# Kernel optimization log

Measured on AMD Instinct MI355X. Metric: run time of the kernel, lower is better.

The kernel has to match this reference:

```python
import jax, jax.numpy as jnp
import numpy as np


def setup_inputs() -> dict:
    key = jax.random.key(0)
    B, S = 8, 4096
    MAX_SEQ_LEN = 4096
    D_MODEL = 1024
    # ids are float in [0, max_seq_len); original module casts int ids to float anyway
    input_ids = jax.random.uniform(key, (B, S), dtype=jnp.float32) * MAX_SEQ_LEN
    return {"input_ids": input_ids, "max_seq_len": MAX_SEQ_LEN, "d_model": D_MODEL}


def reference(input_ids, max_seq_len, d_model):
    # Normalize ids from [0, max_seq_len] to [-1, 1] (Chebyshev domain).
    x = 2.0 * input_ids.astype(jnp.float32) / max_seq_len - 1.0  # [B, S]
    t0 = jnp.ones_like(x)  # T_0(x) = 1
    t1 = x                  # T_1(x) = x

    def step(carry, _):
        t_prev, t_cur = carry
        t_next = 2.0 * x * t_cur - t_prev
        return (t_cur, t_next), t_next

    _, rest = jax.lax.scan(step, (t0, t1), None, length=d_model - 2)
    # rest: [d_model-2, B, S]
    emb = jnp.concatenate([t0[None], t1[None], rest], axis=0)  # [d_model, B, S]
    return jnp.moveaxis(emb, 0, -1)  # [B, S, d_model]
```

## Files before the change

### kernel.cpp

```cpp
#include <hip/hip_runtime.h>
#include <hip/hip_bf16.h>

__global__ void __launch_bounds__(256)
cheb_kernel(const float* __restrict__ ids,
            const int* __restrict__ p_maxlen,
            float* __restrict__ out,
            int n_rows, int d_model) {
    const float inv = 2.0f / (float)(*p_maxlen);
    const int per_row = d_model >> 3;
    const long long total = (long long)n_rows * per_row;
    const long long stride = (long long)gridDim.x * blockDim.x;
    for (long long tid = (long long)blockIdx.x * blockDim.x + threadIdx.x;
         tid < total; tid += stride) {
        const int row = (int)(tid / per_row);
        const int seg = (int)(tid - (long long)row * per_row);

        float x = fmaf(ids[row], inv, -1.0f);
        x = fminf(fmaxf(x, -1.0f), 1.0f);
        const float sx = sqrtf(fmaxf(0.0f, 1.0f - x * x));
        const float theta = acosf(x);

        const int n0 = seg << 3;
        float c, s;
        sincosf((float)n0 * theta, &s, &c);

        float v[8];
#pragma unroll
        for (int k = 0; k < 8; ++k) {
            v[k] = c;
            const float nc = fmaf(c, x, -(s * sx));
            const float ns = fmaf(s, x,  (c * sx));
            c = nc; s = ns;
        }

        float4* o = (float4*)(out + tid * 8);
        o[0] = make_float4(v[0], v[1], v[2], v[3]);
        o[1] = make_float4(v[4], v[5], v[6], v[7]);
    }
}

extern "C" void kernel_launch(void* const* d_in, const int* in_sizes, int n_in,
                              void* d_out, int out_size, void* d_ws, size_t ws_size,
                              hipStream_t stream) {
    const float* ids     = (const float*)d_in[0];
    const int*   pmaxlen = (const int*)d_in[1];
    float*       out     = (float*)d_out;

    const int n_rows  = in_sizes[0];
    const int d_model = out_size / n_rows;

    const long long total = (long long)n_rows * (d_model >> 3);
    int blocks = (int)((total + 255) / 256);
    if (blocks > 16384) blocks = 16384;

    cheb_kernel<<<blocks, 256, 0, stream>>>(ids, pmaxlen, out, n_rows, d_model);
}
```

Baseline: 31.22 us.

## Specialize d_model=1024 path with one wave per row and coalesced stores

Adds a kernel specialized for d_model=1024. Each wavefront handles one row, and each lane writes float4s at lane-contiguous addresses across four 256-element chunks, so stores are fully coalesced. The base angles come from the hardware sin/cos instructions on revolution-scaled, range-reduced inputs, and a rotation recurrence steps between chunks instead of calling sincosf per segment. This trades some accuracy from the native trig and the longer recurrence for cheaper math and better store patterns. Other d_model values fall back to the generic kernel.

```diff
diff --git a/kernel.cpp b/kernel.cpp
--- a/kernel.cpp
+++ b/kernel.cpp
@@ -1,11 +1,57 @@
 #include <hip/hip_runtime.h>
 #include <hip/hip_bf16.h>
 
+#define INV2PI 0.15915494309189535f
+
 __global__ void __launch_bounds__(256)
-cheb_kernel(const float* __restrict__ ids,
-            const int* __restrict__ p_maxlen,
-            float* __restrict__ out,
-            int n_rows, int d_model) {
+cheb1024_kernel(const float* __restrict__ ids,
+                const int* __restrict__ p_maxlen,
+                float* __restrict__ out,
+                int n_rows) {
+    const float inv = 2.0f / (float)(*p_maxlen);
+    const int wave = threadIdx.x >> 6;
+    const int lane = threadIdx.x & 63;
+    const int row  = blockIdx.x * 4 + wave;
+    if (row >= n_rows) return;
+
+    float x = fmaf(ids[row], inv, -1.0f);
+    x = fminf(fmaxf(x, -1.0f), 1.0f);
+    const float sx = sqrtf(fmaxf(0.0f, 1.0f - x * x));
+    const float trev = acosf(x) * INV2PI;
+
+    float brev = (float)(4 * lane) * trev;
+    brev -= floorf(brev);
+    float bc = __builtin_amdgcn_cosf(brev);
+    float bs = __builtin_amdgcn_sinf(brev);
+
+    float crev = 256.0f * trev;
+    crev -= floorf(crev);
+    const float C = __builtin_amdgcn_cosf(crev);
+    const float S = __builtin_amdgcn_sinf(crev);
+
+    float* rowp = out + (size_t)row * 1024;
+#pragma unroll
+    for (int q = 0; q < 4; ++q) {
+        const float v0 = bc;
+        const float c1 = fmaf(bc, x, -(bs * sx));
+        const float s1 = fmaf(bs, x,  (bc * sx));
+        const float c2 = fmaf(c1, x, -(s1 * sx));
+        const float s2 = fmaf(s1, x,  (c1 * sx));
+        const float c3 = fmaf(c2, x, -(s2 * sx));
+
+        ((float4*)(rowp + q * 256))[lane] = make_float4(v0, c1, c2, c3);
+
+        const float nbc = fmaf(bc, C, -(bs * S));
+        const float nbs = fmaf(bs, C,  (bc * S));
+        bc = nbc; bs = nbs;
+    }
+}
+
+__global__ void __launch_bounds__(256)
+cheb_generic_kernel(const float* __restrict__ ids,
+                    const int* __restrict__ p_maxlen,
+                    float* __restrict__ out,
+                    int n_rows, int d_model) {
     const float inv = 2.0f / (float)(*p_maxlen);
     const int per_row = d_model >> 3;
     const long long total = (long long)n_rows * per_row;
@@ -20,9 +66,8 @@
         const float sx = sqrtf(fmaxf(0.0f, 1.0f - x * x));
         const float theta = acosf(x);
 
-        const int n0 = seg << 3;
         float c, s;
-        sincosf((float)n0 * theta, &s, &c);
+        sincosf((float)(seg << 3) * theta, &s, &c);
 
         float v[8];
 #pragma unroll
@@ -32,7 +77,6 @@
             const float ns = fmaf(s, x,  (c * sx));
             c = nc; s = ns;
         }
-
         float4* o = (float4*)(out + tid * 8);
         o[0] = make_float4(v[0], v[1], v[2], v[3]);
         o[1] = make_float4(v[4], v[5], v[6], v[7]);
@@ -49,9 +93,13 @@
     const int n_rows  = in_sizes[0];
     const int d_model = out_size / n_rows;
 
-    const long long total = (long long)n_rows * (d_model >> 3);
-    int blocks = (int)((total + 255) / 256);
-    if (blocks > 16384) blocks = 16384;
-
-    cheb_kernel<<<blocks, 256, 0, stream>>>(ids, pmaxlen, out, n_rows, d_model);
+    if (d_model == 1024) {
+        const int blocks = (n_rows + 3) / 4;
+        cheb1024_kernel<<<blocks, 256, 0, stream>>>(ids, pmaxlen, out, n_rows);
+    } else {
+        const long long total = (long long)n_rows * (d_model >> 3);
+        int blocks = (int)((total + 255) / 256);
+        if (blocks > 16384) blocks = 16384;
+        cheb_generic_kernel<<<blocks, 256, 0, stream>>>(ids, pmaxlen, out, n_rows, d_model);
+    }
 }
```

New measurement: 26.40 us. -15.4%, faster.
